# Optimization experiments

Measured on AMD Instinct MI355X. Metric: run time of the kernel, lower is better.

The kernel has to match this reference:

```python
import jax, jax.numpy as jnp
import numpy as np

N = 100000   # nodes
E = 1600000  # edges (avg degree 16)
D = 30       # in channels
H = 4        # attention heads
C = 30       # per-head out channels
EPS = 1e-5
NEG_SLOPE = 0.2


def setup_inputs() -> dict:
    ks = jax.random.split(jax.random.key(0), 12)
    s = 0.1
    return {
        "h": jax.random.normal(ks[0], (N, D), jnp.float32),
        "edge_index": jax.random.randint(ks[1], (2, E), 0, N),
        "edge_weight": jax.random.uniform(ks[2], (E,), jnp.float32),
        "bn_gamma": jnp.ones((D,), jnp.float32),
        "bn_beta": jnp.zeros((D,), jnp.float32),
        "W": jax.random.normal(ks[3], (D, H * C), jnp.float32) * s,
        "att_src": jax.random.normal(ks[4], (H, C), jnp.float32) * s,
        "att_dst": jax.random.normal(ks[5], (H, C), jnp.float32) * s,
        "att_edge": jax.random.normal(ks[6], (H, C), jnp.float32) * s,
        "W_edge": jax.random.normal(ks[7], (1, H * C), jnp.float32) * s,
        "bias": jnp.zeros((C,), jnp.float32),
        "fc1_w": jax.random.normal(ks[8], (C, C), jnp.float32) * s,
        "fc1_b": jnp.zeros((C,), jnp.float32),
        "fc2_w": jax.random.normal(ks[9], (C, C), jnp.float32) * s,
        "fc2_b": jnp.zeros((C,), jnp.float32),
        "fc3_w": jax.random.normal(ks[10], (C, C), jnp.float32) * s,
        "fc3_b": jnp.zeros((C,), jnp.float32),
    }


def reference(h, edge_index, edge_weight, bn_gamma, bn_beta, W, att_src, att_dst,
              att_edge, W_edge, bias, fc1_w, fc1_b, fc2_w, fc2_b, fc3_w, fc3_b):
    n = h.shape[0]
    # BatchNorm1d, training-mode batch statistics (biased variance)
    mu = h.mean(0)
    var = ((h - mu) ** 2).mean(0)
    hn = (h - mu) * jax.lax.rsqrt(var + EPS) * bn_gamma + bn_beta

    # GATConv with add_self_loops=True; self-loop edge_attr = mean edge weight
    # (PyG fill_value='mean' default)
    loop = jnp.arange(n)
    src = jnp.concatenate([edge_index[0], loop])
    dst = jnp.concatenate([edge_index[1], loop])
    ew = jnp.concatenate([edge_weight, jnp.full((n,), edge_weight.mean(), h.dtype)])

    x = (hn @ W).reshape(n, H, C)                    # [N,H,C] shared src/dst lin
    a_src = (x * att_src).sum(-1)                    # [N,H]
    a_dst = (x * att_dst).sum(-1)                    # [N,H]
    e = (ew[:, None] * W_edge[0]).reshape(-1, H, C)  # [E2,H,C] lin_edge (no bias)
    a_edge = (e * att_edge).sum(-1)                  # [E2,H]

    alpha = jax.nn.leaky_relu(a_src[src] + a_dst[dst] + a_edge, NEG_SLOPE)
    # scatter-softmax over incoming edges of each destination node
    m = jax.ops.segment_max(alpha, dst, num_segments=n)
    ex = jnp.exp(alpha - m[dst])
    den = jax.ops.segment_sum(ex, dst, num_segments=n)
    alpha = ex / (den[dst] + 1e-16)                  # [E2,H]

    out = jax.ops.segment_sum(x[src] * alpha[:, :, None], dst, num_segments=n)
    out = out.mean(1) + bias                         # concat=False -> head mean

    out = jax.nn.relu(out)
    out = jax.nn.relu(out @ fc1_w.T + fc1_b)
    out = jax.nn.relu(out @ fc2_w.T + fc2_b)
    return out @ fc3_w.T + fc3_b
```

## Files before the change

kernel.cpp:

```cpp
#include <hip/hip_runtime.h>
#include <hip/hip_fp16.h>

#define N_NODES 100000
#define N_EDGES 1600000
#define D_IN 30
#define H_HEADS 4
#define C_OUT 30
#define EPSV 1e-5f
#define NEG 0.2f
#define MAXDEG 48
#define NPB 64
#define NBUCK 256
#define BUCK_NODES 391
#define SLICE_CAP 48
#define EPB 4096
#define BIN_BLOCKS ((N_EDGES + EPB - 1) / EPB)
#define STATS_BLOCKS 224
#define X_BLOCKS ((N_NODES + NPB - 1) / NPB)
#define NODE_BLOCKS (N_NODES / 16)

#define OFF_XH    0
#define OFF_ADST  6400000
#define OFF_PAR   6800000
#define OFF_DEG   6804096
#define OFF_STATS 6904256
#define OFF_BCNTG 6904320
#define OFF_ADJ   7004416
#define OFF_GBUF  11804416
#define OFF_PERM  21413632

__device__ __forceinline__ float hb2f(unsigned int bits) {
    __half_raw r; r.x = (unsigned short)bits;
    return __half2float(*reinterpret_cast<__half*>(&r));
}

__global__ __launch_bounds__(512) void k_bin(const int* __restrict__ ei,
                                             const float* __restrict__ ew,
                                             const float* __restrict__ h,
                                             unsigned int* __restrict__ bcnt_g,
                                             uint2* __restrict__ gbuf,
                                             float* __restrict__ stats) {
    int t = threadIdx.x;
    if (blockIdx.x < BIN_BLOCKS) {
        __shared__ int bcnt[NBUCK];
        if (t < NBUCK) bcnt[t] = 0;
        __syncthreads();
        int blk = blockIdx.x;
        int j0 = blk * EPB + t;
#pragma unroll
        for (int r = 0; r < 8; ++r) {
            int j = j0 + r * 512;
            if (j < N_EDGES) {
                int s = __builtin_nontemporal_load(ei + j);
                int d = __builtin_nontemporal_load(ei + N_EDGES + j);
                float w = __builtin_nontemporal_load(ew + j);
                __half hv = __float2half_rn(w);
                unsigned short hb = *reinterpret_cast<unsigned short*>(&hv);
                unsigned lo = ((unsigned)s << 15) | (unsigned)(hb & 0x7FFFu);
                int b = d / BUCK_NODES;
                int rank = atomicAdd(&bcnt[b], 1);
                if (rank < SLICE_CAP)
                    gbuf[((size_t)b * BIN_BLOCKS + blk) * SLICE_CAP + rank] =
                        make_uint2(lo, (unsigned)d);
            }
        }
        __syncthreads();
        if (t < NBUCK) bcnt_g[(size_t)blk * NBUCK + t] = (unsigned)bcnt[t];
        return;
    }
    __shared__ float ls[61];
    if (t < 61) ls[t] = 0.f;
    __syncthreads();
    float s[D_IN], q[D_IN];
#pragma unroll
    for (int d = 0; d < D_IN; ++d) { s[d] = 0.f; q[d] = 0.f; }
    int idx0 = (blockIdx.x - BIN_BLOCKS) * 512 + t;
    int stride = STATS_BLOCKS * 512;
    for (int r = idx0; r < N_NODES; r += stride) {
        const float* row = h + r * D_IN;
#pragma unroll
        for (int d = 0; d < D_IN; ++d) { float v = row[d]; s[d] += v; q[d] += v * v; }
    }
    float es = 0.f;
    for (int i = idx0; i < N_EDGES; i += stride) es += ew[i];
#pragma unroll
    for (int d = 0; d < D_IN; ++d) {
        for (int off = 32; off; off >>= 1) {
            s[d] += __shfl_down(s[d], off);
            q[d] += __shfl_down(q[d], off);
        }
    }
    for (int off = 32; off; off >>= 1) es += __shfl_down(es, off);
    if ((t & 63) == 0) {
#pragma unroll
        for (int d = 0; d < D_IN; ++d) { atomicAdd(&ls[d], s[d]); atomicAdd(&ls[30 + d], q[d]); }
        atomicAdd(&ls[60], es);
    }
    __syncthreads();
    if (t < 61) atomicAdd(&stats[t], ls[t]);
}

__global__ __launch_bounds__(256) void k_bx(const unsigned int* __restrict__ bcnt_g,
                                            const uint2* __restrict__ gbuf,
                                            unsigned int* __restrict__ adj,
                                            int* __restrict__ deg,
                                            int* __restrict__ perm,
                                            const float* __restrict__ h,
                                            const float* __restrict__ W,
                                            const float* __restrict__ Wedge,
                                            const float* __restrict__ att_edge,
                                            const float* __restrict__ att_src,
                                            const float* __restrict__ att_dst,
                                            const float* __restrict__ gamma,
                                            const float* __restrict__ beta,
                                            const float* __restrict__ stats,
                                            float* __restrict__ par,
                                            unsigned int* __restrict__ xh,
                                            float* __restrict__ adst) {
    __shared__ __align__(16) unsigned char smem[38816];
    int t = threadIdx.x;
    if (blockIdx.x < 2 * NBUCK) {
        unsigned* rows = (unsigned*)smem;
        int* cnt = (int*)(smem + 37632);
        int* hist = (int*)(smem + 38416);
        int* pfx  = (int*)(smem + 38612);
        int bb = blockIdx.x;
        int b = bb >> 1, half = bb & 1;
        int lo = b * BUCK_NODES + half * 196;
        int span = half ? (BUCK_NODES - 196) : 196;
        int lim = N_NODES - lo; if (lim > span) lim = span; if (lim < 0) lim = 0;
        for (int i = t; i < 196; i += 256) cnt[i] = 0;
        if (t < 49) hist[t] = 0;
        __syncthreads();
        const uint2* brec = gbuf + (size_t)b * BIN_BLOCKS * SLICE_CAP;
        int totslots = BIN_BLOCKS * SLICE_CAP;
        for (int i = t; i < totslots; i += 256) {
            int sl = i / SLICE_CAP;
            int r = i - sl * SLICE_CAP;
            unsigned c = bcnt_g[(size_t)sl * NBUCK + b];
            if (r < (int)c) {
                uint2 rec = brec[i];
                int li = (int)rec.y - lo;
                if (li >= 0 && li < lim) {
                    int p = atomicAdd(&cnt[li], 1);
                    if (p < MAXDEG) rows[li * MAXDEG + p] = rec.x;
                }
            }
        }
        __syncthreads();
        int tot = lim * MAXDEG;
        for (int i = t; i < tot; i += 256) {
            int li = i / MAXDEG;
            int p = i - li * MAXDEG;
            if (p < cnt[li]) adj[(size_t)lo * MAXDEG + i] = rows[i];
        }
        for (int i = t; i < lim; i += 256) {
            int c = cnt[i]; c = (c > MAXDEG) ? MAXDEG : c;
            deg[lo + i] = c;
            atomicAdd(&hist[c], 1);
        }
        __syncthreads();
        if (t == 0) {
            int acc = 0;
            for (int kk = MAXDEG; kk >= 0; --kk) { pfx[kk] = acc; acc += hist[kk]; }
        }
        __syncthreads();
        for (int i = t; i < lim; i += 256) {
            int c = cnt[i]; c = (c > MAXDEG) ? MAXDEG : c;
            int r = atomicAdd(&pfx[c], 1);
            perm[lo + r] = lo + i;
        }
        return;
    }
    float* W2s = (float*)smem;
    float* hs  = (float*)(smem + 14400);
    float* psd = (float*)(smem + 22080);
    float* cq  = (float*)(smem + 23040);
    float* b2s = (float*)(smem + 23072);
    float* scs = (float*)(smem + 23552);
    float* shs = (float*)(smem + 23672);
    int bx = blockIdx.x - 2 * NBUCK;
    if (t < D_IN) {
        float mu = stats[t] * (1.f / N_NODES);
        float var = stats[30 + t] * (1.f / N_NODES) - mu * mu;
        float inv = 1.f / sqrtf(var + EPSV);
        float sc = gamma[t] * inv;
        scs[t] = sc; shs[t] = beta[t] - mu * sc;
    }
    __syncthreads();
    {
        const float4* W4 = (const float4*)W;
        for (int i = t; i < 900; i += 256) {
            float4 w4 = W4[i];
            float sc = scs[(i * 4) / 120];
            w4.x *= sc; w4.y *= sc; w4.z *= sc; w4.w *= sc;
            *(float4*)&W2s[i * 4] = w4;
        }
    }
    if (t >= 128 && t < 248) {
        int c = t - 128;
        float b = 0.f;
#pragma unroll
        for (int d = 0; d < D_IN; ++d) b = fmaf(shs[d], W[d * 120 + c], b);
        b2s[c] = b;
    }
    if (bx == 0 && t >= 248 && t < 252) {
        int hh = t - 248;
        float k = 0.f;
        for (int c = 0; c < 30; ++c) k = fmaf(Wedge[hh * 30 + c], att_edge[hh * 30 + c], k);
        par[64 + hh] = k;
    }
    if (bx == 0 && t == 252) par[68] = stats[60] * (1.f / N_EDGES);
    __syncthreads();
    int base = bx * NPB;
    int cnt2 = N_NODES - base; if (cnt2 > NPB) cnt2 = NPB;
    if (t < 240) {
        int d = t >> 3, q = t & 7, hh = q & 3;
        const float* att = (q < 4) ? att_src : att_dst;
        float sum = 0.f;
#pragma unroll
        for (int c = 0; c < 30; ++c) sum = fmaf(W2s[d * 120 + hh * 30 + c], att[hh * 30 + c], sum);
        psd[t] = sum;
    }
    if (t >= 240 && t < 248) {
        int q = t - 240, hh = q & 3;
        const float* att = (q < 4) ? att_src : att_dst;
        float sum = 0.f;
#pragma unroll
        for (int c = 0; c < 30; ++c) sum = fmaf(b2s[hh * 30 + c], att[hh * 30 + c], sum);
        cq[q] = sum;
    }
    {
        const float4* h4 = (const float4*)(h + (size_t)base * 30);
        int n4 = (cnt2 * 30) >> 2;
        for (int i = t; i < n4; i += 256) ((float4*)hs)[i] = h4[i];
    }
    __syncthreads();
    const float2* W2p = (const float2*)W2s;
    int total = cnt2 * 60;
    for (int o = t; o < total; o += 256) {
        int node = o / 60, p = o - node * 60;
        const float* hrow = hs + node * 30;
        float ax = b2s[2 * p], ay = b2s[2 * p + 1];
        const float2* Wp = W2p + p;
#pragma unroll
        for (int d = 0; d < 30; ++d) {
            float hv = hrow[d];
            float2 w = Wp[d * 60];
            ax = fmaf(hv, w.x, ax);
            ay = fmaf(hv, w.y, ay);
        }
        __half2 pk = __float22half2_rn(make_float2(ax, ay));
        int hh = p / 15, j = p - hh * 15;
        xh[(size_t)(base + node) * 64 + hh * 16 + j] = *reinterpret_cast<unsigned int*>(&pk);
    }
    for (int v = t; v < cnt2 * 8; v += 256) {
        int node = v >> 3, q = v & 7;
        const float* hrow = hs + node * 30;
        float sum = cq[q];
#pragma unroll
        for (int d = 0; d < 30; ++d) sum = fmaf(hrow[d], psd[d * 8 + q], sum);
        int n = base + node;
        if (q < 4) xh[(size_t)n * 64 + q * 16 + 15] = __float_as_uint(sum);
        else       adst[n * H_HEADS + (q - 4)] = sum;
    }
}

__global__ __launch_bounds__(256) void k_node(const uint4* __restrict__ xh4,
                                              const float* __restrict__ adst,
                                              const float* __restrict__ par,
                                              const int* __restrict__ deg,
                                              const unsigned int* __restrict__ adj,
                                              const int* __restrict__ perm,
                                              const float* __restrict__ bias,
                                              const float* __restrict__ fc1w,
                                              const float* __restrict__ fc1b,
                                              const float* __restrict__ fc2w,
                                              const float* __restrict__ fc2b,
                                              const float* __restrict__ fc3w,
                                              const float* __restrict__ fc3b,
                                              float* __restrict__ out) {
    __shared__ float Ws[3][900];
    __shared__ float Bs[3][30];
    __shared__ float bias_s[32];
    __shared__ float tb[16 * 32];
    __shared__ int nids[16];
    int t = threadIdx.x;
    {
        const float4* s0 = (const float4*)fc1w;
        const float4* s1 = (const float4*)fc2w;
        const float4* s2 = (const float4*)fc3w;
        for (int i = t; i < 225; i += 256) {
            *(float4*)&Ws[0][i * 4] = s0[i];
            *(float4*)&Ws[1][i * 4] = s1[i];
            *(float4*)&Ws[2][i * 4] = s2[i];
        }
    }
    if (t < 30) { Bs[0][t] = fc1b[t]; Bs[1][t] = fc2b[t]; Bs[2][t] = fc3b[t]; }
    if (t < 32) bias_s[t] = (t < 30) ? bias[t] : 0.f;
    __syncthreads();

    int l = t & 63;
    int k = l & 15;
    int wv = t >> 6;
    int q = (l >> 4) & 3;
    int nl = wv * 4 + q;
    int n = perm[blockIdx.x * 16 + nl];
    if (k == 0) nids[nl] = n;
    int h = k >> 2;
    int asl_b = (((l & 48) | (k & 12) | 3) << 2);
    int pb4 = (l & 48) << 2;

    float kh = par[64 + h];
    float ew_mean = par[68];
    float adn = adst[n * H_HEADS + h];

    int dn = min(deg[n], MAXDEG);
    int dmax = dn;
    dmax = max(dmax, __shfl_xor(dmax, 16));
    dmax = max(dmax, __shfl_xor(dmax, 32));

    const unsigned int* arow = adj + (size_t)n * MAXDEG;
    unsigned int aw0 = arow[k];
    unsigned int aw1 = 0, aw2 = 0;
    if (dmax > 16) aw1 = arow[16 + k];
    if (dmax > 32) aw2 = arow[32 + k];

    uint4 rw = xh4[(unsigned)n * 16u + (unsigned)k];
    float asn = __uint_as_float((unsigned)__builtin_amdgcn_ds_bpermute(asl_b, (int)rw.w));
    float z = fmaf(ew_mean, kh, adn) + asn;
    z = fmaxf(z, NEG * z);
    float e0 = __expf(z);
    float den = e0;
    float2 x0 = __half22float2(*(const __half2*)&rw.x);
    float2 x1 = __half22float2(*(const __half2*)&rw.y);
    float2 x2 = __half22float2(*(const __half2*)&rw.z);
    float2 x3 = __half22float2(*(const __half2*)&rw.w);
    float2 a0 = make_float2(e0 * x0.x, e0 * x0.y);
    float2 a1 = make_float2(e0 * x1.x, e0 * x1.y);
    float2 a2 = make_float2(e0 * x2.x, e0 * x2.y);
    float2 a3 = make_float2(e0 * x3.x, e0 * x3.y);

    for (int u0 = 0; u0 < dmax; u0 += 4) {
        unsigned ed[4], ss[4];
        uint4 rr[4];
#pragma unroll
        for (int v = 0; v < 4; ++v) {
            int u = u0 + v;
            unsigned int aw = (u < 16) ? aw0 : ((u < 32) ? aw1 : aw2);
            ed[v] = (unsigned)__builtin_amdgcn_ds_bpermute(pb4 + ((u & 15) << 2), (int)aw);
            ss[v] = (u < dn) ? (ed[v] >> 15) : (unsigned)n;
        }
#pragma unroll
        for (int v = 0; v < 4; ++v) rr[v] = xh4[(size_t)ss[v] * 16u + (unsigned)k];
#pragma unroll
        for (int v = 0; v < 4; ++v) {
            int u = u0 + v;
            bool valid = (u < dn);
            float w = hb2f(ed[v] & 0x7FFFu);
            float as_ = __uint_as_float((unsigned)__builtin_amdgcn_ds_bpermute(asl_b, (int)rr[v].w));
            float zz = fmaf(w, kh, adn) + as_;
            zz = fmaxf(zz, NEG * zz);
            float ee = __expf(zz);
            ee = valid ? ee : 0.f;
            den += ee;
            float2 y0 = __half22float2(*(const __half2*)&rr[v].x);
            float2 y1 = __half22float2(*(const __half2*)&rr[v].y);
            float2 y2 = __half22float2(*(const __half2*)&rr[v].z);
            float2 y3 = __half22float2(*(const __half2*)&rr[v].w);
            a0.x = fmaf(ee, y0.x, a0.x); a0.y = fmaf(ee, y0.y, a0.y);
            a1.x = fmaf(ee, y1.x, a1.x); a1.y = fmaf(ee, y1.y, a1.y);
            a2.x = fmaf(ee, y2.x, a2.x); a2.y = fmaf(ee, y2.y, a2.y);
            a3.x = fmaf(ee, y3.x, a3.x); a3.y = fmaf(ee, y3.y, a3.y);
        }
    }

    float rden = 0.25f / (den + 1e-16f);
    a0.x *= rden; a0.y *= rden; a1.x *= rden; a1.y *= rden;
    a2.x *= rden; a2.y *= rden; a3.x *= rden; a3.y *= rden;

    a0.x += __shfl_xor(a0.x, 4); a0.y += __shfl_xor(a0.y, 4);
    a1.x += __shfl_xor(a1.x, 4); a1.y += __shfl_xor(a1.y, 4);
    a2.x += __shfl_xor(a2.x, 4); a2.y += __shfl_xor(a2.y, 4);
    a3.x += __shfl_xor(a3.x, 4); a3.y += __shfl_xor(a3.y, 4);
    a0.x += __shfl_xor(a0.x, 8); a0.y += __shfl_xor(a0.y, 8);
    a1.x += __shfl_xor(a1.x, 8); a1.y += __shfl_xor(a1.y, 8);
    a2.x += __shfl_xor(a2.x, 8); a2.y += __shfl_xor(a2.y, 8);
    a3.x += __shfl_xor(a3.x, 8); a3.y += __shfl_xor(a3.y, 8);

    if ((k & 12) == 0) {
        int ch = k * 8;
        float v0 = fmaxf(a0.x + bias_s[ch + 0], 0.f);
        float v1 = fmaxf(a0.y + bias_s[ch + 1], 0.f);
        float v2 = fmaxf(a1.x + bias_s[ch + 2], 0.f);
        float v3 = fmaxf(a1.y + bias_s[ch + 3], 0.f);
        float v4 = fmaxf(a2.x + bias_s[ch + 4], 0.f);
        float v5 = fmaxf(a2.y + bias_s[ch + 5], 0.f);
        float v6 = fmaxf(a3.x + bias_s[ch + 6], 0.f);
        float v7 = fmaxf(a3.y + bias_s[ch + 7], 0.f);
        float* p = tb + nl * 32 + ch;
        *(float4*)p       = make_float4(v0, v1, v2, v3);
        *(float4*)(p + 4) = make_float4(v4, v5, v6, v7);
    }
    __syncthreads();

    for (int lay = 0; lay < 3; ++lay) {
        float y[2];
#pragma unroll
        for (int j = 0; j < 2; ++j) {
            int i = t + j * 256;
            int nd = i >> 5, c = i & 31;
            y[j] = 0.f;
            if (c < 30) {
                float acc = Bs[lay][c];
                const float* Wl = &Ws[lay][c * 30];
                const float* tr = &tb[nd * 32];
#pragma unroll
                for (int cc = 0; cc < 30; ++cc) acc = fmaf(tr[cc], Wl[cc], acc);
                y[j] = (lay < 2) ? fmaxf(acc, 0.f) : acc;
            }
        }
        __syncthreads();
#pragma unroll
        for (int j = 0; j < 2; ++j) {
            int i = t + j * 256;
            int nd = i >> 5, c = i & 31;
            if (c < 30) {
                if (lay < 2) tb[nd * 32 + c] = y[j];
                else out[(size_t)nids[nd] * 30 + c] = y[j];
            }
        }
        if (lay < 2) __syncthreads();
    }
}

extern "C" void kernel_launch(void* const* d_in, const int* in_sizes, int n_in,
                              void* d_out, int out_size, void* d_ws, size_t ws_size,
                              hipStream_t stream) {
    const float* h        = (const float*)d_in[0];
    const int*   ei       = (const int*)d_in[1];
    const float* ew       = (const float*)d_in[2];
    const float* gamma    = (const float*)d_in[3];
    const float* beta     = (const float*)d_in[4];
    const float* W        = (const float*)d_in[5];
    const float* att_src  = (const float*)d_in[6];
    const float* att_dst  = (const float*)d_in[7];
    const float* att_edge = (const float*)d_in[8];
    const float* Wedge    = (const float*)d_in[9];
    const float* bias     = (const float*)d_in[10];
    const float* fc1w     = (const float*)d_in[11];
    const float* fc1b     = (const float*)d_in[12];
    const float* fc2w     = (const float*)d_in[13];
    const float* fc2b     = (const float*)d_in[14];
    const float* fc3w     = (const float*)d_in[15];
    const float* fc3b     = (const float*)d_in[16];

    float*        ws     = (float*)d_ws;
    unsigned int* xh     = (unsigned int*)(ws + OFF_XH);
    float*        adstb  = ws + OFF_ADST;
    float*        par    = ws + OFF_PAR;
    float*        stats  = ws + OFF_STATS;
    int*          deg    = (int*)(ws + OFF_DEG);
    unsigned int* bcnt_g = (unsigned int*)(ws + OFF_BCNTG);
    unsigned int* adj    = (unsigned int*)(ws + OFF_ADJ);
    uint2*        gbuf   = (uint2*)(ws + OFF_GBUF);
    int*          perm   = (int*)(ws + OFF_PERM);
    float*        out    = (float*)d_out;

    hipMemsetAsync(stats, 0, 64 * 4, stream);

    k_bin<<<BIN_BLOCKS + STATS_BLOCKS, 512, 0, stream>>>(ei, ew, h, bcnt_g, gbuf, stats);
    k_bx<<<2 * NBUCK + X_BLOCKS, 256, 0, stream>>>(bcnt_g, gbuf, adj, deg, perm, h, W,
                                                   Wedge, att_edge, att_src, att_dst,
                                                   gamma, beta, stats, par, xh, adstb);
    k_node<<<NODE_BLOCKS, 256, 0, stream>>>((const uint4*)xh, adstb, par, deg, adj, perm,
                                            bias, fc1w, fc1b, fc2w, fc2b, fc3w, fc3b, out);
}
```

Baseline: 172.1 us.

## Double-buffer neighbor gathers, use finer buckets, fuse edge-weight sum into binning

The node kernel now issues the next group of four neighbor gathers before it consumes the current group, with two register buffers alternating. This hides global-load latency behind the softmax and accumulate math, at the cost of more registers. Binning moves from 256 buckets split in two halves to 512 buckets of 196 nodes with half the slice capacity. Each build block now reads only its own records, where before each half-bucket block scanned all of its bucket's records. The edge-weight sum moves from the stats blocks into the binning blocks, which already load each weight, so the second full pass over edge weights is gone. Risk: halving SLICE_CAP to 24 may drop edges from crowded slices.

```diff
diff --git a/kernel.cpp b/kernel.cpp
--- a/kernel.cpp
+++ b/kernel.cpp
@@ -10,9 +10,10 @@
 #define NEG 0.2f
 #define MAXDEG 48
 #define NPB 64
-#define NBUCK 256
-#define BUCK_NODES 391
-#define SLICE_CAP 48
+#define NBUCK 512
+#define BUCK_NODES 196
+#define BUILD_BLOCKS 511
+#define SLICE_CAP 24
 #define EPB 4096
 #define BIN_BLOCKS ((N_EDGES + EPB - 1) / EPB)
 #define STATS_BLOCKS 224
@@ -25,9 +26,9 @@
 #define OFF_DEG   6804096
 #define OFF_STATS 6904256
 #define OFF_BCNTG 6904320
-#define OFF_ADJ   7004416
-#define OFF_GBUF  11804416
-#define OFF_PERM  21413632
+#define OFF_ADJ   7105024
+#define OFF_GBUF  11905024
+#define OFF_PERM  21514240
 
 __device__ __forceinline__ float hb2f(unsigned int bits) {
     __half_raw r; r.x = (unsigned short)bits;
@@ -43,10 +44,11 @@
     int t = threadIdx.x;
     if (blockIdx.x < BIN_BLOCKS) {
         __shared__ int bcnt[NBUCK];
-        if (t < NBUCK) bcnt[t] = 0;
+        bcnt[t] = 0;
         __syncthreads();
         int blk = blockIdx.x;
         int j0 = blk * EPB + t;
+        float es = 0.f;
 #pragma unroll
         for (int r = 0; r < 8; ++r) {
             int j = j0 + r * 512;
@@ -54,6 +56,7 @@
                 int s = __builtin_nontemporal_load(ei + j);
                 int d = __builtin_nontemporal_load(ei + N_EDGES + j);
                 float w = __builtin_nontemporal_load(ew + j);
+                es += w;
                 __half hv = __float2half_rn(w);
                 unsigned short hb = *reinterpret_cast<unsigned short*>(&hv);
                 unsigned lo = ((unsigned)s << 15) | (unsigned)(hb & 0x7FFFu);
@@ -64,12 +67,14 @@
                         make_uint2(lo, (unsigned)d);
             }
         }
-        __syncthreads();
-        if (t < NBUCK) bcnt_g[(size_t)blk * NBUCK + t] = (unsigned)bcnt[t];
+        for (int off = 32; off; off >>= 1) es += __shfl_down(es, off);
+        if ((t & 63) == 0) atomicAdd(&stats[60], es);
+        __syncthreads();
+        bcnt_g[(size_t)blk * NBUCK + t] = (unsigned)bcnt[t];
         return;
     }
-    __shared__ float ls[61];
-    if (t < 61) ls[t] = 0.f;
+    __shared__ float ls[60];
+    if (t < 60) ls[t] = 0.f;
     __syncthreads();
     float s[D_IN], q[D_IN];
 #pragma unroll
@@ -81,8 +86,6 @@
 #pragma unroll
         for (int d = 0; d < D_IN; ++d) { float v = row[d]; s[d] += v; q[d] += v * v; }
     }
-    float es = 0.f;
-    for (int i = idx0; i < N_EDGES; i += stride) es += ew[i];
 #pragma unroll
     for (int d = 0; d < D_IN; ++d) {
         for (int off = 32; off; off >>= 1) {
@@ -90,14 +93,12 @@
             q[d] += __shfl_down(q[d], off);
         }
     }
-    for (int off = 32; off; off >>= 1) es += __shfl_down(es, off);
     if ((t & 63) == 0) {
 #pragma unroll
         for (int d = 0; d < D_IN; ++d) { atomicAdd(&ls[d], s[d]); atomicAdd(&ls[30 + d], q[d]); }
-        atomicAdd(&ls[60], es);
-    }
-    __syncthreads();
-    if (t < 61) atomicAdd(&stats[t], ls[t]);
+    }
+    __syncthreads();
+    if (t < 60) atomicAdd(&stats[t], ls[t]);
 }
 
 __global__ __launch_bounds__(256) void k_bx(const unsigned int* __restrict__ bcnt_g,
@@ -119,17 +120,15 @@
                                             float* __restrict__ adst) {
     __shared__ __align__(16) unsigned char smem[38816];
     int t = threadIdx.x;
-    if (blockIdx.x < 2 * NBUCK) {
+    if (blockIdx.x < BUILD_BLOCKS) {
         unsigned* rows = (unsigned*)smem;
         int* cnt = (int*)(smem + 37632);
         int* hist = (int*)(smem + 38416);
         int* pfx  = (int*)(smem + 38612);
-        int bb = blockIdx.x;
-        int b = bb >> 1, half = bb & 1;
-        int lo = b * BUCK_NODES + half * 196;
-        int span = half ? (BUCK_NODES - 196) : 196;
-        int lim = N_NODES - lo; if (lim > span) lim = span; if (lim < 0) lim = 0;
-        for (int i = t; i < 196; i += 256) cnt[i] = 0;
+        int b = blockIdx.x;
+        int lo = b * BUCK_NODES;
+        int lim = N_NODES - lo; if (lim > BUCK_NODES) lim = BUCK_NODES;
+        for (int i = t; i < BUCK_NODES; i += 256) cnt[i] = 0;
         if (t < 49) hist[t] = 0;
         __syncthreads();
         const uint2* brec = gbuf + (size_t)b * BIN_BLOCKS * SLICE_CAP;
@@ -141,10 +140,8 @@
             if (r < (int)c) {
                 uint2 rec = brec[i];
                 int li = (int)rec.y - lo;
-                if (li >= 0 && li < lim) {
-                    int p = atomicAdd(&cnt[li], 1);
-                    if (p < MAXDEG) rows[li * MAXDEG + p] = rec.x;
-                }
+                int p = atomicAdd(&cnt[li], 1);
+                if (p < MAXDEG) rows[li * MAXDEG + p] = rec.x;
             }
         }
         __syncthreads();
@@ -179,7 +176,7 @@
     float* b2s = (float*)(smem + 23072);
     float* scs = (float*)(smem + 23552);
     float* shs = (float*)(smem + 23672);
-    int bx = blockIdx.x - 2 * NBUCK;
+    int bx = blockIdx.x - BUILD_BLOCKS;
     if (t < D_IN) {
         float mu = stats[t] * (1.f / N_NODES);
         float var = stats[30 + t] * (1.f / N_NODES) - mu * mu;
@@ -264,6 +261,41 @@
         if (q < 4) xh[(size_t)n * 64 + q * 16 + 15] = __float_as_uint(sum);
         else       adst[n * H_HEADS + (q - 4)] = sum;
     }
+}
+
+#define GISSUE(U0, ED, RR) {                                                    \
+    unsigned ss_[4];                                                            \
+    _Pragma("unroll")                                                           \
+    for (int v = 0; v < 4; ++v) {                                               \
+        int u = (U0) + v;                                                       \
+        unsigned aw = (u < 16) ? aw0 : ((u < 32) ? aw1 : aw2);                  \
+        ED[v] = (unsigned)__builtin_amdgcn_ds_bpermute(pb4 + ((u & 15) << 2), (int)aw); \
+        ss_[v] = (u < dn) ? (ED[v] >> 15) : (unsigned)n;                        \
+    }                                                                           \
+    _Pragma("unroll")                                                           \
+    for (int v = 0; v < 4; ++v) RR[v] = xh4[(size_t)ss_[v] * 16u + (unsigned)k]; \
+}
+
+#define GCONSUME(U0, ED, RR) {                                                  \
+    _Pragma("unroll")                                                           \
+    for (int v = 0; v < 4; ++v) {                                               \
+        int u = (U0) + v;                                                       \
+        bool valid = (u < dn);                                                  \
+        float w = hb2f(ED[v] & 0x7FFFu);                                        \
+        float as_ = __uint_as_float((unsigned)__builtin_amdgcn_ds_bpermute(asl_b, (int)RR[v].w)); \
+        float zz = fmaf(w, kh, adn) + as_;                                      \
+        zz = fmaxf(zz, NEG * zz);                                               \
+        float ee = valid ? __expf(zz) : 0.f;                                    \
+        den += ee;                                                              \
+        float2 y0 = __half22float2(*(const __half2*)&RR[v].x);                  \
+        float2 y1 = __half22float2(*(const __half2*)&RR[v].y);                  \
+        float2 y2 = __half22float2(*(const __half2*)&RR[v].z);                  \
+        float2 y3 = __half22float2(*(const __half2*)&RR[v].w);                  \
+        a0.x = fmaf(ee, y0.x, a0.x); a0.y = fmaf(ee, y0.y, a0.y);               \
+        a1.x = fmaf(ee, y1.x, a1.x); a1.y = fmaf(ee, y1.y, a1.y);               \
+        a2.x = fmaf(ee, y2.x, a2.x); a2.y = fmaf(ee, y2.y, a2.y);               \
+        a3.x = fmaf(ee, y3.x, a3.x); a3.y = fmaf(ee, y3.y, a3.y);               \
+    }                                                                           \
 }
 
 __global__ __launch_bounds__(256) void k_node(const uint4* __restrict__ xh4,
@@ -341,37 +373,21 @@
     float2 a2 = make_float2(e0 * x2.x, e0 * x2.y);
     float2 a3 = make_float2(e0 * x3.x, e0 * x3.y);
 
-    for (int u0 = 0; u0 < dmax; u0 += 4) {
-        unsigned ed[4], ss[4];
-        uint4 rr[4];
-#pragma unroll
-        for (int v = 0; v < 4; ++v) {
-            int u = u0 + v;
-            unsigned int aw = (u < 16) ? aw0 : ((u < 32) ? aw1 : aw2);
-            ed[v] = (unsigned)__builtin_amdgcn_ds_bpermute(pb4 + ((u & 15) << 2), (int)aw);
-            ss[v] = (u < dn) ? (ed[v] >> 15) : (unsigned)n;
-        }
-#pragma unroll
-        for (int v = 0; v < 4; ++v) rr[v] = xh4[(size_t)ss[v] * 16u + (unsigned)k];
-#pragma unroll
-        for (int v = 0; v < 4; ++v) {
-            int u = u0 + v;
-            bool valid = (u < dn);
-            float w = hb2f(ed[v] & 0x7FFFu);
-            float as_ = __uint_as_float((unsigned)__builtin_amdgcn_ds_bpermute(asl_b, (int)rr[v].w));
-            float zz = fmaf(w, kh, adn) + as_;
-            zz = fmaxf(zz, NEG * zz);
-            float ee = __expf(zz);
-            ee = valid ? ee : 0.f;
-            den += ee;
-            float2 y0 = __half22float2(*(const __half2*)&rr[v].x);
-            float2 y1 = __half22float2(*(const __half2*)&rr[v].y);
-            float2 y2 = __half22float2(*(const __half2*)&rr[v].z);
-            float2 y3 = __half22float2(*(const __half2*)&rr[v].w);
-            a0.x = fmaf(ee, y0.x, a0.x); a0.y = fmaf(ee, y0.y, a0.y);
-            a1.x = fmaf(ee, y1.x, a1.x); a1.y = fmaf(ee, y1.y, a1.y);
-            a2.x = fmaf(ee, y2.x, a2.x); a2.y = fmaf(ee, y2.y, a2.y);
-            a3.x = fmaf(ee, y3.x, a3.x); a3.y = fmaf(ee, y3.y, a3.y);
+    if (dmax > 0) {
+        unsigned edA[4], edB[4];
+        uint4 rrA[4], rrB[4];
+        GISSUE(0, edA, rrA);
+        int u0 = 0;
+        while (true) {
+            bool moreB = (u0 + 4 < dmax);
+            if (moreB) GISSUE(u0 + 4, edB, rrB);
+            GCONSUME(u0, edA, rrA);
+            if (!moreB) break;
+            bool moreA = (u0 + 8 < dmax);
+            if (moreA) GISSUE(u0 + 8, edA, rrA);
+            GCONSUME(u0 + 4, edB, rrB);
+            if (!moreA) break;
+            u0 += 8;
         }
     }
 
@@ -470,9 +486,9 @@
     hipMemsetAsync(stats, 0, 64 * 4, stream);
 
     k_bin<<<BIN_BLOCKS + STATS_BLOCKS, 512, 0, stream>>>(ei, ew, h, bcnt_g, gbuf, stats);
-    k_bx<<<2 * NBUCK + X_BLOCKS, 256, 0, stream>>>(bcnt_g, gbuf, adj, deg, perm, h, W,
-                                                   Wedge, att_edge, att_src, att_dst,
-                                                   gamma, beta, stats, par, xh, adstb);
+    k_bx<<<BUILD_BLOCKS + X_BLOCKS, 256, 0, stream>>>(bcnt_g, gbuf, adj, deg, perm, h, W,
+                                                      Wedge, att_edge, att_src, att_dst,
+                                                      gamma, beta, stats, par, xh, adstb);
     k_node<<<NODE_BLOCKS, 256, 0, stream>>>((const uint4*)xh, adstb, par, deg, adj, perm,
                                             bias, fc1w, fc1b, fc2w, fc2b, fc3w, fc3b, out);
 }
```

Result: slower. 190.3 us (+10.6%).
